# Performance work log

Hardware: AMD Instinct MI355X
Metric: run time of the kernel (lower is better)

The kernel has to match this reference:

```python
import jax, jax.numpy as jnp
import numpy as np

# Config (matches AttentionConfig)
B, T, D = 2, 2048, 2048
H, KV, HD = 32, 8, 64          # n_heads, n_kv_heads, head_dim = d_model // n_heads
GROUPS = H // KV               # 4 query heads share each KV head
THETA = 10000.0
SCALE = 1.0 / np.sqrt(HD)
EPS = 1e-6


def setup_inputs() -> dict:
    key = jax.random.key(0)
    ks = jax.random.split(key, 6)
    def xavier(k, fan_in, fan_out):
        limit = np.sqrt(6.0 / (fan_in + fan_out))
        return jax.random.uniform(k, (fan_in, fan_out), jnp.float32, -limit, limit)
    return {
        "x": jax.random.normal(ks[0], (B, T, D), jnp.float32),
        "Wq": xavier(ks[1], D, H * HD),
        "Wk": xavier(ks[2], D, KV * HD),
        "Wv": xavier(ks[3], D, KV * HD),
        "Wo": xavier(ks[4], H * HD, D),
        "q_scale": jnp.ones((HD,), jnp.float32),
        "k_scale": jnp.ones((HD,), jnp.float32),
    }


def _rmsnorm(x, scale):
    # per-head RMSNorm over last dim (head_dim)
    rms = jnp.sqrt(jnp.mean(jnp.square(x), axis=-1, keepdims=True) + EPS)
    return (x / rms) * scale


def _rope(x):
    # x: (B, T, h, HD); rotate-half RoPE, offset=0
    pos = jnp.arange(x.shape[1], dtype=jnp.float32)
    inv_freq = 1.0 / (THETA ** (jnp.arange(0, HD, 2, dtype=jnp.float32) / HD))
    ang = pos[:, None] * inv_freq[None, :]          # (T, HD/2)
    cos = jnp.cos(ang)[None, :, None, :]
    sin = jnp.sin(ang)[None, :, None, :]
    x1, x2 = x[..., : HD // 2], x[..., HD // 2 :]
    return jnp.concatenate([x1 * cos - x2 * sin, x2 * cos + x1 * sin], axis=-1)


def reference(x, Wq, Wk, Wv, Wo, q_scale, k_scale):
    # projections -> (B, T, heads, HD)
    q = (x @ Wq).reshape(B, T, H, HD)
    k = (x @ Wk).reshape(B, T, KV, HD)
    v = (x @ Wv).reshape(B, T, KV, HD)
    # per-head QK RMSNorm (applied before RoPE, as in the module)
    q = _rmsnorm(q, q_scale)
    k = _rmsnorm(k, k_scale)
    # RoPE on q and k
    q = _rope(q)
    k = _rope(k)
    # repeat KV heads: head index = kv_head * GROUPS + g (matches _repeat_kv)
    k = jnp.repeat(k, GROUPS, axis=2)   # (B, T, H, HD)
    v = jnp.repeat(v, GROUPS, axis=2)
    # attention scores (B, H, T, T)
    logits = jnp.einsum("bqhd,bkhd->bhqk", q, k) * SCALE
    causal = jnp.triu(jnp.ones((T, T), bool), k=1)  # True = masked
    logits = jnp.where(causal[None, None], -jnp.inf, logits)
    w = jax.nn.softmax(logits, axis=-1)
    w = jnp.nan_to_num(w)
    out = jnp.einsum("bhqk,bkhd->bqhd", w, v).reshape(B, T, H * HD)
    return out @ Wo
```

## Files before the change

kernel.cpp:

```cpp
#include <hip/hip_runtime.h>
#include <hip/hip_bf16.h>

typedef __attribute__((ext_vector_type(4))) float f32x4;
typedef __attribute__((ext_vector_type(8))) short bf16x8;
typedef __attribute__((ext_vector_type(4))) short short4v;

#define DEVI __device__ __forceinline__

constexpr int Bc = 2, Tc = 2048, Dc = 2048, Hc = 32, KVc = 8, HDc = 64;
constexpr int GRP = Hc / KVc;
constexpr float EPSc = 1e-6f;
constexpr float QMULT = 0.125f * 1.4426950408889634f;
constexpr float INV2PI = 0.15915494309189535f;
constexpr float ROPE_C = 0.41524101186092029f;

DEVI short f2b(float f) {
    __hip_bfloat16 h = __float2bfloat16(f);
    short s;
    __builtin_memcpy(&s, &h, sizeof(short));
    return s;
}
DEVI float b2f(short s) {
    unsigned int u = ((unsigned int)(unsigned short)s) << 16;
    float f;
    __builtin_memcpy(&f, &u, sizeof(float));
    return f;
}

#define GLOAD16(g, l)                                                        \
    __builtin_amdgcn_global_load_lds(                                        \
        (const __attribute__((address_space(1))) void*)(g),                  \
        (__attribute__((address_space(3))) void*)(l), 16, 0, 0)

__global__ __launch_bounds__(256) void prep_all(const float* __restrict__ x,
                                                const float* __restrict__ Wq,
                                                const float* __restrict__ Wk,
                                                const float* __restrict__ Wv,
                                                const float* __restrict__ Wo,
                                                short* __restrict__ xb,
                                                short* __restrict__ WqkvT,
                                                short* __restrict__ WoT) {
    const int z = blockIdx.z;
    if (z == 4) {
        size_t base = ((size_t)(blockIdx.y * 32 + blockIdx.x) * 256 + threadIdx.x) * 8;
#pragma unroll
        for (int p = 0; p < 4; ++p) {
            size_t i = base + (size_t)p * 2097152;
            float4 a = *reinterpret_cast<const float4*>(x + i);
            float4 b = *reinterpret_cast<const float4*>(x + i + 4);
            bf16x8 o = {f2b(a.x), f2b(a.y), f2b(a.z), f2b(a.w),
                        f2b(b.x), f2b(b.y), f2b(b.z), f2b(b.w)};
            *reinterpret_cast<bf16x8*>(xb + i) = o;
        }
        return;
    }
    const float* src;
    short* dst;
    int C;
    if (z == 0)      { src = Wq; dst = WqkvT;                          C = 2048; }
    else if (z == 1) { src = Wk; dst = WqkvT + (size_t)2048 * 2048;    C = 512; }
    else if (z == 2) { src = Wv; dst = WqkvT + (size_t)2560 * 2048;    C = 512; }
    else             { src = Wo; dst = WoT;                            C = 2048; }
    const int n0 = blockIdx.x * 64, k0 = blockIdx.y * 64;
    if (n0 >= C) return;

    __shared__ __align__(16) short t[64][72];
    const int rl = threadIdx.x >> 2, q = threadIdx.x & 3;
#pragma unroll
    for (int jj = 0; jj < 4; ++jj) {
        float4 v = *reinterpret_cast<const float4*>(src + (size_t)(k0 + rl) * C + n0 + q * 16 + jj * 4);
        short4v s = {f2b(v.x), f2b(v.y), f2b(v.z), f2b(v.w)};
        *reinterpret_cast<short4v*>(&t[rl][q * 16 + jj * 4]) = s;
    }
    __syncthreads();
    alignas(16) short buf[16];
#pragma unroll
    for (int e = 0; e < 16; ++e) buf[e] = t[q * 16 + e][rl];
    short* d = dst + (size_t)(n0 + rl) * 2048 + k0 + q * 16;
    *reinterpret_cast<int4*>(d) = reinterpret_cast<int4*>(buf)[0];
    *reinterpret_cast<int4*>(d + 8) = reinterpret_cast<int4*>(buf)[1];
}

DEVI void xcd_swizzle(int nx, int& bx, int& by) {
    int nwg = nx * gridDim.y;
    int fb = by * nx + bx;
    int cpx = nwg >> 3;
    int swz = (fb & 7) * cpx + (fb >> 3);
    by = swz / nx;
    bx = swz - by * nx;
}

__global__ __launch_bounds__(256) void gemm_proj(const short* __restrict__ A,
                                                 const short* __restrict__ Bt,
                                                 const float* __restrict__ qs,
                                                 const float* __restrict__ ks,
                                                 short* __restrict__ qb,
                                                 short* __restrict__ kb,
                                                 short* __restrict__ vslab) {
    constexpr int K = 2048;
    __shared__ __align__(16) short sA[2][128 * 64];
    __shared__ __align__(16) short sB[2][128 * 64];

    const int tid = threadIdx.x;
    const int wave = tid >> 6, lane = tid & 63;
    const int lhi = lane >> 4, llo = lane & 15;
    int bx = blockIdx.x, by = blockIdx.y;
    xcd_swizzle(24, bx, by);
    const int bm = by * 128, bn = bx * 128;
    const int wm = (wave >> 1) * 64, wn = (wave & 1) * 64;

    const short* apt[4];
    const short* bpt[4];
#pragma unroll
    for (int l = 0; l < 4; ++l) {
        int c = l * 256 + tid;
        int r = c >> 3, ck = (c & 7) ^ (r & 7);
        apt[l] = A + (size_t)(bm + r) * K + ck * 8;
        bpt[l] = Bt + (size_t)(bn + r) * K + ck * 8;
    }

    f32x4 acc[4][4] = {};

#pragma unroll
    for (int l = 0; l < 4; ++l) {
        GLOAD16(apt[l], &sA[0][(l * 256 + tid) * 8]);
        GLOAD16(bpt[l], &sB[0][(l * 256 + tid) * 8]);
    }
    int c = 0;
    const int co0 = ((lhi ^ (llo & 7)) << 3);
    const int co1 = (((4 + lhi) ^ (llo & 7)) << 3);

#pragma unroll 1
    for (int k0 = 0; k0 < K; k0 += 64) {
        if (k0 + 64 < K) {
            const int kn = k0 + 64;
#pragma unroll
            for (int l = 0; l < 4; ++l) {
                GLOAD16(apt[l] + kn, &sA[c ^ 1][(l * 256 + tid) * 8]);
                GLOAD16(bpt[l] + kn, &sB[c ^ 1][(l * 256 + tid) * 8]);
            }
            asm volatile("s_waitcnt vmcnt(8)" ::: "memory");
        } else {
            asm volatile("s_waitcnt vmcnt(0)" ::: "memory");
        }
        __builtin_amdgcn_s_barrier();
        asm volatile("" ::: "memory");

#pragma unroll
        for (int kk = 0; kk < 2; ++kk) {
            const int co = kk ? co1 : co0;
            bf16x8 af[4], bf[4];
#pragma unroll
            for (int i = 0; i < 4; ++i)
                af[i] = *reinterpret_cast<const bf16x8*>(&sA[c][(wm + i * 16 + llo) * 64 + co]);
#pragma unroll
            for (int j = 0; j < 4; ++j)
                bf[j] = *reinterpret_cast<const bf16x8*>(&sB[c][(wn + j * 16 + llo) * 64 + co]);
#pragma unroll
            for (int i = 0; i < 4; ++i)
#pragma unroll
                for (int j = 0; j < 4; ++j)
                    acc[i][j] = __builtin_amdgcn_mfma_f32_16x16x32_bf16(af[i], bf[j], acc[i][j], 0, 0, 0);
        }

        asm volatile("" ::: "memory");
        __builtin_amdgcn_s_barrier();
        c ^= 1;
    }

    const int rm = bm + wm;
    const int b = rm >> 11;
    const int tb = rm & 2047;
    const int col0 = bn + wn;

    if (col0 < 2560) {
        const bool isq = col0 < 2048;
        const float* scale = isq ? qs : ks;
        const float mult = isq ? QMULT : 1.0f;
        float scl[4];
#pragma unroll
        for (int j = 0; j < 4; ++j) scl[j] = scale[j * 16 + llo];
        short* outp;
        if (isq)
            outp = qb + (size_t)(b * Hc + (col0 >> 6)) * 2048 * 64;
        else
            outp = kb + (size_t)(b * KVc + ((col0 - 2048) >> 6)) * 2048 * 64;
        const float ir0 = INV2PI * exp2f(-ROPE_C * (float)llo);
        const float ir1 = INV2PI * exp2f(-ROPE_C * (float)(16 + llo));
#pragma unroll
        for (int i = 0; i < 4; ++i)
#pragma unroll
            for (int r = 0; r < 4; ++r) {
                float ss = 0.f;
#pragma unroll
                for (int j = 0; j < 4; ++j) ss += acc[i][j][r] * acc[i][j][r];
                ss += __shfl_xor(ss, 1);
                ss += __shfl_xor(ss, 2);
                ss += __shfl_xor(ss, 4);
                ss += __shfl_xor(ss, 8);
                float rinv = 1.0f / sqrtf(ss * (1.0f / 64.0f) + EPSc);
                float vn[4];
#pragma unroll
                for (int j = 0; j < 4; ++j) vn[j] = acc[i][j][r] * rinv * scl[j];
                const int t = tb + i * 16 + lhi * 4 + r;
                float f0 = (float)t * ir0;
                f0 -= floorf(f0);
                float f1 = (float)t * ir1;
                f1 -= floorf(f1);
                float sn0 = __builtin_amdgcn_sinf(f0), cs0 = __builtin_amdgcn_cosf(f0);
                float sn1 = __builtin_amdgcn_sinf(f1), cs1 = __builtin_amdgcn_cosf(f1);
                size_t base = (size_t)t * 64 + llo;
                outp[base]      = f2b((vn[0] * cs0 - vn[2] * sn0) * mult);
                outp[base + 16] = f2b((vn[1] * cs1 - vn[3] * sn1) * mult);
                outp[base + 32] = f2b((vn[2] * cs0 + vn[0] * sn0) * mult);
                outp[base + 48] = f2b((vn[3] * cs1 + vn[1] * sn1) * mult);
            }
    } else {
        const int cb = col0 - 2560;
#pragma unroll
        for (int i = 0; i < 4; ++i)
#pragma unroll
            for (int j = 0; j < 4; ++j)
#pragma unroll
                for (int r = 0; r < 4; ++r)
                    vslab[(size_t)(rm + i * 16 + lhi * 4 + r) * 512 + cb + j * 16 + llo] =
                        f2b(acc[i][j][r]);
    }
}

template <typename CT>
__global__ __launch_bounds__(256) void gemm_bt(const short* __restrict__ A,
                                               const short* __restrict__ Bt,
                                               CT* __restrict__ C, int M, int N, int K) {
    __shared__ __align__(16) short sA[2][128 * 64];
    __shared__ __align__(16) short sB[2][128 * 64];

    const int tid = threadIdx.x;
    const int wave = tid >> 6, lane = tid & 63;
    const int lhi = lane >> 4, llo = lane & 15;
    int bx = blockIdx.x, by = blockIdx.y;
    xcd_swizzle(gridDim.x, bx, by);
    const int bm = by * 128, bn = bx * 128;
    const int wm = (wave >> 1) * 64, wn = (wave & 1) * 64;

    const short* apt[4];
    const short* bpt[4];
#pragma unroll
    for (int l = 0; l < 4; ++l) {
        int c = l * 256 + tid;
        int r = c >> 3, ck = (c & 7) ^ (r & 7);
        apt[l] = A + (size_t)(bm + r) * K + ck * 8;
        bpt[l] = Bt + (size_t)(bn + r) * K + ck * 8;
    }

    f32x4 acc[4][4] = {};

#pragma unroll
    for (int l = 0; l < 4; ++l) {
        GLOAD16(apt[l], &sA[0][(l * 256 + tid) * 8]);
        GLOAD16(bpt[l], &sB[0][(l * 256 + tid) * 8]);
    }
    int c = 0;
    const int co0 = ((lhi ^ (llo & 7)) << 3);
    const int co1 = (((4 + lhi) ^ (llo & 7)) << 3);

#pragma unroll 1
    for (int k0 = 0; k0 < K; k0 += 64) {
        if (k0 + 64 < K) {
            const int kn = k0 + 64;
#pragma unroll
            for (int l = 0; l < 4; ++l) {
                GLOAD16(apt[l] + kn, &sA[c ^ 1][(l * 256 + tid) * 8]);
                GLOAD16(bpt[l] + kn, &sB[c ^ 1][(l * 256 + tid) * 8]);
            }
            asm volatile("s_waitcnt vmcnt(8)" ::: "memory");
        } else {
            asm volatile("s_waitcnt vmcnt(0)" ::: "memory");
        }
        __builtin_amdgcn_s_barrier();
        asm volatile("" ::: "memory");

#pragma unroll
        for (int kk = 0; kk < 2; ++kk) {
            const int co = kk ? co1 : co0;
            bf16x8 af[4], bf[4];
#pragma unroll
            for (int i = 0; i < 4; ++i)
                af[i] = *reinterpret_cast<const bf16x8*>(&sA[c][(wm + i * 16 + llo) * 64 + co]);
#pragma unroll
            for (int j = 0; j < 4; ++j)
                bf[j] = *reinterpret_cast<const bf16x8*>(&sB[c][(wn + j * 16 + llo) * 64 + co]);
#pragma unroll
            for (int i = 0; i < 4; ++i)
#pragma unroll
                for (int j = 0; j < 4; ++j)
                    acc[i][j] = __builtin_amdgcn_mfma_f32_16x16x32_bf16(af[i], bf[j], acc[i][j], 0, 0, 0);
        }

        asm volatile("" ::: "memory");
        __builtin_amdgcn_s_barrier();
        c ^= 1;
    }

#pragma unroll
    for (int i = 0; i < 4; ++i)
#pragma unroll
        for (int j = 0; j < 4; ++j)
#pragma unroll
            for (int r = 0; r < 4; ++r) {
                size_t idx = (size_t)(bm + wm + i * 16 + lhi * 4 + r) * N + bn + wn + j * 16 + llo;
                if constexpr (sizeof(CT) == 2)
                    C[idx] = f2b(acc[i][j][r]);
                else
                    C[idx] = acc[i][j][r];
            }
}

__global__ __launch_bounds__(256) void fuse_vt(const short* __restrict__ vsrc,
                                               short* __restrict__ vt, int ldin) {
    __shared__ __align__(16) short t[64][72];
    const int tile = blockIdx.x, kv = blockIdx.y, b = blockIdx.z;
    const int tl = threadIdx.x >> 2, q = threadIdx.x & 3;
    const short* src = vsrc + (size_t)(b * 2048 + tile * 64 + tl) * ldin + kv * 64 + q * 16;
    *reinterpret_cast<bf16x8*>(&t[tl][q * 16]) = *reinterpret_cast<const bf16x8*>(src);
    *reinterpret_cast<bf16x8*>(&t[tl][q * 16 + 8]) = *reinterpret_cast<const bf16x8*>(src + 8);
    __syncthreads();
    alignas(16) short buf[16];
#pragma unroll
    for (int e = 0; e < 16; ++e) buf[e] = t[q * 16 + e][tl];
    short* dst = vt + ((size_t)(b * 8 + kv) * 32 + tile) * 4096 + tl * 64 + q * 16;
    *reinterpret_cast<int4*>(dst) = reinterpret_cast<int4*>(buf)[0];
    *reinterpret_cast<int4*>(dst + 8) = reinterpret_cast<int4*>(buf)[1];
}

__global__ __launch_bounds__(256) void attn_fwd(const short* __restrict__ Qb,
                                                const short* __restrict__ Kb,
                                                const short* __restrict__ Vt,
                                                short* __restrict__ Ob) {
    __shared__ __align__(16) short sK[2][64 * 64];
    __shared__ __align__(16) short sV[2][64 * 64];
    __shared__ __align__(16) short sP[4][32 * 72];

    const int pair = blockIdx.x;
    const int h = blockIdx.y, b = blockIdx.z;
    const int kvh = h >> 2;
    const int tid = threadIdx.x, wave = tid >> 6, lane = tid & 63;
    const int lhi = lane >> 4, llo = lane & 15;

    const short* Qp = Qb + (size_t)(b * Hc + h) * Tc * 64;
    const short* Kp = Kb + (size_t)(b * KVc + kvh) * Tc * 64;
    const short* Vp = Vt + (size_t)(b * KVc + kvh) * 32 * 4096;

    const int srow0 = tid >> 3, sslot0 = tid & 7;
    const int srow1 = (256 + tid) >> 3, sslot1 = tid & 7;
    const int soff0 = (sslot0 ^ (srow0 & 7)) * 8;
    const int soff1 = (sslot1 ^ (srow1 & 7)) * 8;

#pragma unroll 1
    for (int sub = 0; sub < 2; ++sub) {
        const int qt = sub ? pair : 15 - pair;
        const int Q0 = qt * 128 + wave * 32;
        const int ktmax_w = (Q0 + 31) >> 6;
        const int nkt = 2 * qt + 2;

        bf16x8 qf[2][2];
#pragma unroll
        for (int q16 = 0; q16 < 2; ++q16)
#pragma unroll
            for (int kk = 0; kk < 2; ++kk)
                qf[q16][kk] = *reinterpret_cast<const bf16x8*>(
                    Qp + (size_t)(Q0 + q16 * 16 + llo) * 64 + kk * 32 + lhi * 8);

        f32x4 o[2][4] = {};
        float mreg[2] = {-1e30f, -1e30f};
        float lreg[2] = {0.f, 0.f};

        {
            GLOAD16(Kp + (size_t)srow0 * 64 + soff0, &sK[0][tid * 8]);
            GLOAD16(Vp + (size_t)srow0 * 64 + soff0, &sV[0][tid * 8]);
            GLOAD16(Kp + (size_t)srow1 * 64 + soff1, &sK[0][(256 + tid) * 8]);
            GLOAD16(Vp + (size_t)srow1 * 64 + soff1, &sV[0][(256 + tid) * 8]);
        }
        int c = 0;

#pragma unroll 1
        for (int kt = 0; kt < nkt; ++kt) {
            const bool has_next = (kt + 1) < nkt;
            if (has_next) {
                const size_t kbase = (size_t)(kt + 1) * 4096;
                GLOAD16(Kp + kbase + srow0 * 64 + soff0, &sK[c ^ 1][tid * 8]);
                GLOAD16(Vp + kbase + srow0 * 64 + soff0, &sV[c ^ 1][tid * 8]);
                GLOAD16(Kp + kbase + srow1 * 64 + soff1, &sK[c ^ 1][(256 + tid) * 8]);
                GLOAD16(Vp + kbase + srow1 * 64 + soff1, &sV[c ^ 1][(256 + tid) * 8]);
                asm volatile("s_waitcnt vmcnt(4)" ::: "memory");
            } else {
                asm volatile("s_waitcnt vmcnt(0)" ::: "memory");
            }
            __builtin_amdgcn_s_barrier();
            asm volatile("" ::: "memory");

            if (kt <= ktmax_w) {
                const short* sKc = sK[c];
                const short* sVc = sV[c];
                f32x4 st[2][4];
#pragma unroll
                for (int n = 0; n < 4; ++n) {
                    int krow = n * 16 + llo;
                    bf16x8 ka0 = *reinterpret_cast<const bf16x8*>(
                        &sKc[krow * 64 + ((lhi ^ (krow & 7)) << 3)]);
                    bf16x8 ka1 = *reinterpret_cast<const bf16x8*>(
                        &sKc[krow * 64 + (((4 + lhi) ^ (krow & 7)) << 3)]);
                    f32x4 z = {0.f, 0.f, 0.f, 0.f};
                    st[0][n] = __builtin_amdgcn_mfma_f32_16x16x32_bf16(ka0, qf[0][0], z, 0, 0, 0);
                    st[0][n] = __builtin_amdgcn_mfma_f32_16x16x32_bf16(ka1, qf[0][1], st[0][n], 0, 0, 0);
                    st[1][n] = __builtin_amdgcn_mfma_f32_16x16x32_bf16(ka0, qf[1][0], z, 0, 0, 0);
                    st[1][n] = __builtin_amdgcn_mfma_f32_16x16x32_bf16(ka1, qf[1][1], st[1][n], 0, 0, 0);
                }
                if (kt == ktmax_w) {
#pragma unroll
                    for (int q16 = 0; q16 < 2; ++q16) {
                        int qg = Q0 + q16 * 16 + llo;
#pragma unroll
                        for (int n = 0; n < 4; ++n)
#pragma unroll
                            for (int r = 0; r < 4; ++r) {
                                int kvg = kt * 64 + n * 16 + lhi * 4 + r;
                                if (kvg > qg) st[q16][n][r] = -1e30f;
                            }
                    }
                }
                float pm[2];
#pragma unroll
                for (int q16 = 0; q16 < 2; ++q16) {
                    float p = st[q16][0][0];
#pragma unroll
                    for (int n = 0; n < 4; ++n)
#pragma unroll
                        for (int r = 0; r < 4; ++r) p = fmaxf(p, st[q16][n][r]);
                    p = fmaxf(p, __shfl_xor(p, 16));
                    p = fmaxf(p, __shfl_xor(p, 32));
                    pm[q16] = p;
                }
                bool defer = __all((pm[0] - mreg[0] <= 8.f) && (pm[1] - mreg[1] <= 8.f));
                if (!defer) {
                    float alpha[2];
#pragma unroll
                    for (int q16 = 0; q16 < 2; ++q16) {
                        float mn = fmaxf(mreg[q16], pm[q16]);
                        alpha[q16] = __builtin_amdgcn_exp2f(mreg[q16] - mn);
                        mreg[q16] = mn;
                        lreg[q16] *= alpha[q16];
                    }
#pragma unroll
                    for (int q16 = 0; q16 < 2; ++q16)
#pragma unroll
                        for (int r = 0; r < 4; ++r) {
                            float ar = __shfl(alpha[q16], lhi * 4 + r);
#pragma unroll
                            for (int j = 0; j < 4; ++j) o[q16][j][r] *= ar;
                        }
                }
#pragma unroll
                for (int q16 = 0; q16 < 2; ++q16) {
                    float ps = 0.f;
#pragma unroll
                    for (int n = 0; n < 4; ++n)
#pragma unroll
                        for (int r = 0; r < 4; ++r) {
                            float p = __builtin_amdgcn_exp2f(st[q16][n][r] - mreg[q16]);
                            st[q16][n][r] = p;
                            ps += p;
                        }
                    ps += __shfl_xor(ps, 16);
                    ps += __shfl_xor(ps, 32);
                    lreg[q16] += ps;
                }
#pragma unroll
                for (int q16 = 0; q16 < 2; ++q16)
#pragma unroll
                    for (int n = 0; n < 4; ++n) {
                        short4v p4 = {f2b(st[q16][n][0]), f2b(st[q16][n][1]),
                                      f2b(st[q16][n][2]), f2b(st[q16][n][3])};
                        *reinterpret_cast<short4v*>(
                            &sP[wave][(q16 * 16 + llo) * 72 + n * 16 + lhi * 4]) = p4;
                    }
#pragma unroll
                for (int kk = 0; kk < 2; ++kk) {
                    bf16x8 pa0 = *reinterpret_cast<const bf16x8*>(
                        &sP[wave][(0 * 16 + llo) * 72 + kk * 32 + lhi * 8]);
                    bf16x8 pa1 = *reinterpret_cast<const bf16x8*>(
                        &sP[wave][(1 * 16 + llo) * 72 + kk * 32 + lhi * 8]);
#pragma unroll
                    for (int j = 0; j < 4; ++j) {
                        int vrow = j * 16 + llo;
                        bf16x8 vf = *reinterpret_cast<const bf16x8*>(
                            &sVc[vrow * 64 + ((((kk * 4) + lhi) ^ (vrow & 7)) << 3)]);
                        o[0][j] = __builtin_amdgcn_mfma_f32_16x16x32_bf16(pa0, vf, o[0][j], 0, 0, 0);
                        o[1][j] = __builtin_amdgcn_mfma_f32_16x16x32_bf16(pa1, vf, o[1][j], 0, 0, 0);
                    }
                }
            }
            asm volatile("" ::: "memory");
            __builtin_amdgcn_s_barrier();
            c ^= 1;
        }

#pragma unroll
        for (int q16 = 0; q16 < 2; ++q16) {
            float inv = 1.0f / lreg[q16];
#pragma unroll
            for (int r = 0; r < 4; ++r) {
                float ivr = __shfl(inv, lhi * 4 + r);
                int qrow = Q0 + q16 * 16 + lhi * 4 + r;
#pragma unroll
                for (int j = 0; j < 4; ++j)
                    Ob[((size_t)(b * Tc + qrow)) * 2048 + h * 64 + j * 16 + llo] =
                        f2b(o[q16][j][r] * ivr);
            }
        }
    }
}

extern "C" void kernel_launch(void* const* d_in, const int* in_sizes, int n_in,
                              void* d_out, int out_size, void* d_ws, size_t ws_size,
                              hipStream_t stream) {
    const float* x  = (const float*)d_in[0];
    const float* Wq = (const float*)d_in[1];
    const float* Wk = (const float*)d_in[2];
    const float* Wv = (const float*)d_in[3];
    const float* Wo = (const float*)d_in[4];
    const float* qs = (const float*)d_in[5];
    const float* ks = (const float*)d_in[6];
    float* out = (float*)d_out;

    char* w = (char*)d_ws;
    short* xb    = (short*)(w);
    short* WqkvT = (short*)(w + 16777216);
    short* WoT   = (short*)(w + 29360128);
    short* vslab = (short*)(w + 37748736);
    short* qb    = (short*)(w + 62914560);
    short* kb    = (short*)(w + 79691776);
    short* vt    = WqkvT;
    short* ob    = xb;

    dim3 blk(256);
    prep_all<<<dim3(32, 32, 5), blk, 0, stream>>>(x, Wq, Wk, Wv, Wo, xb, WqkvT, WoT);
    gemm_proj<<<dim3(24, 32), blk, 0, stream>>>(xb, WqkvT, qs, ks, qb, kb, vslab);
    fuse_vt<<<dim3(32, 8, 2), blk, 0, stream>>>(vslab, vt, 512);
    attn_fwd<<<dim3(8, 32, 2), blk, 0, stream>>>(qb, kb, vt, ob);
    gemm_bt<float><<<dim3(16, 32), blk, 0, stream>>>(ob, WoT, out, 4096, 2048, 2048);
}
```

Baseline: 222.8 us.

## Fuse V transpose into projection epilogue, add MFMA priority, tree max reduction

The projection GEMM epilogue now writes V directly in the transposed per-tile layout that attention consumes, so the separate fuse_vt kernel launch and its extra global round trip are removed. The attention kernel raises wave priority around its MFMA blocks with s_setprio, and the row max is computed as a balanced tree instead of a serial chain. The epilogue writes become short4 scattered stores with a stride of 64 elements, which may coalesce poorly.

```diff
diff --git a/kernel.cpp b/kernel.cpp
--- a/kernel.cpp
+++ b/kernel.cpp
@@ -96,7 +96,7 @@
                                                  const float* __restrict__ ks,
                                                  short* __restrict__ qb,
                                                  short* __restrict__ kb,
-                                                 short* __restrict__ vslab) {
+                                                 short* __restrict__ vt) {
     constexpr int K = 2048;
     __shared__ __align__(16) short sA[2][128 * 64];
     __shared__ __align__(16) short sB[2][128 * 64];
@@ -216,15 +216,18 @@
                 outp[base + 48] = f2b((vn[3] * cs1 + vn[1] * sn1) * mult);
             }
     } else {
-        const int cb = col0 - 2560;
+        const int kv = (col0 - 2560) >> 6;
+        const int tile = tb >> 6;
+        short* dst = vt + ((size_t)(b * 8 + kv) * 32 + tile) * 4096;
 #pragma unroll
         for (int i = 0; i < 4; ++i)
 #pragma unroll
-            for (int j = 0; j < 4; ++j)
-#pragma unroll
-                for (int r = 0; r < 4; ++r)
-                    vslab[(size_t)(rm + i * 16 + lhi * 4 + r) * 512 + cb + j * 16 + llo] =
-                        f2b(acc[i][j][r]);
+            for (int j = 0; j < 4; ++j) {
+                short4v p4 = {f2b(acc[i][j][0]), f2b(acc[i][j][1]),
+                              f2b(acc[i][j][2]), f2b(acc[i][j][3])};
+                *reinterpret_cast<short4v*>(
+                    &dst[(j * 16 + llo) * 64 + i * 16 + lhi * 4]) = p4;
+            }
     }
 }
 
@@ -314,23 +317,6 @@
                 else
                     C[idx] = acc[i][j][r];
             }
-}
-
-__global__ __launch_bounds__(256) void fuse_vt(const short* __restrict__ vsrc,
-                                               short* __restrict__ vt, int ldin) {
-    __shared__ __align__(16) short t[64][72];
-    const int tile = blockIdx.x, kv = blockIdx.y, b = blockIdx.z;
-    const int tl = threadIdx.x >> 2, q = threadIdx.x & 3;
-    const short* src = vsrc + (size_t)(b * 2048 + tile * 64 + tl) * ldin + kv * 64 + q * 16;
-    *reinterpret_cast<bf16x8*>(&t[tl][q * 16]) = *reinterpret_cast<const bf16x8*>(src);
-    *reinterpret_cast<bf16x8*>(&t[tl][q * 16 + 8]) = *reinterpret_cast<const bf16x8*>(src + 8);
-    __syncthreads();
-    alignas(16) short buf[16];
-#pragma unroll
-    for (int e = 0; e < 16; ++e) buf[e] = t[q * 16 + e][tl];
-    short* dst = vt + ((size_t)(b * 8 + kv) * 32 + tile) * 4096 + tl * 64 + q * 16;
-    *reinterpret_cast<int4*>(dst) = reinterpret_cast<int4*>(buf)[0];
-    *reinterpret_cast<int4*>(dst + 8) = reinterpret_cast<int4*>(buf)[1];
 }
 
 __global__ __launch_bounds__(256) void attn_fwd(const short* __restrict__ Qb,
@@ -403,6 +389,7 @@
                 const short* sKc = sK[c];
                 const short* sVc = sV[c];
                 f32x4 st[2][4];
+                __builtin_amdgcn_s_setprio(1);
 #pragma unroll
                 for (int n = 0; n < 4; ++n) {
                     int krow = n * 16 + llo;
@@ -416,6 +403,7 @@
                     st[1][n] = __builtin_amdgcn_mfma_f32_16x16x32_bf16(ka0, qf[1][0], z, 0, 0, 0);
                     st[1][n] = __builtin_amdgcn_mfma_f32_16x16x32_bf16(ka1, qf[1][1], st[1][n], 0, 0, 0);
                 }
+                __builtin_amdgcn_s_setprio(0);
                 if (kt == ktmax_w) {
 #pragma unroll
                     for (int q16 = 0; q16 < 2; ++q16) {
@@ -432,11 +420,15 @@
                 float pm[2];
 #pragma unroll
                 for (int q16 = 0; q16 < 2; ++q16) {
-                    float p = st[q16][0][0];
-#pragma unroll
-                    for (int n = 0; n < 4; ++n)
-#pragma unroll
-                        for (int r = 0; r < 4; ++r) p = fmaxf(p, st[q16][n][r]);
+                    float r0 = fmaxf(fmaxf(st[q16][0][0], st[q16][0][1]),
+                                     fmaxf(st[q16][0][2], st[q16][0][3]));
+                    float r1 = fmaxf(fmaxf(st[q16][1][0], st[q16][1][1]),
+                                     fmaxf(st[q16][1][2], st[q16][1][3]));
+                    float r2 = fmaxf(fmaxf(st[q16][2][0], st[q16][2][1]),
+                                     fmaxf(st[q16][2][2], st[q16][2][3]));
+                    float r3 = fmaxf(fmaxf(st[q16][3][0], st[q16][3][1]),
+                                     fmaxf(st[q16][3][2], st[q16][3][3]));
+                    float p = fmaxf(fmaxf(r0, r1), fmaxf(r2, r3));
                     p = fmaxf(p, __shfl_xor(p, 16));
                     p = fmaxf(p, __shfl_xor(p, 32));
                     pm[q16] = p;
@@ -484,6 +476,7 @@
                         *reinterpret_cast<short4v*>(
                             &sP[wave][(q16 * 16 + llo) * 72 + n * 16 + lhi * 4]) = p4;
                     }
+                __builtin_amdgcn_s_setprio(1);
 #pragma unroll
                 for (int kk = 0; kk < 2; ++kk) {
                     bf16x8 pa0 = *reinterpret_cast<const bf16x8*>(
@@ -499,6 +492,7 @@
                         o[1][j] = __builtin_amdgcn_mfma_f32_16x16x32_bf16(pa1, vf, o[1][j], 0, 0, 0);
                     }
                 }
+                __builtin_amdgcn_s_setprio(0);
             }
             asm volatile("" ::: "memory");
             __builtin_amdgcn_s_barrier();
@@ -537,16 +531,14 @@
     short* xb    = (short*)(w);
     short* WqkvT = (short*)(w + 16777216);
     short* WoT   = (short*)(w + 29360128);
-    short* vslab = (short*)(w + 37748736);
+    short* vt    = (short*)(w + 37748736);
     short* qb    = (short*)(w + 62914560);
     short* kb    = (short*)(w + 79691776);
-    short* vt    = WqkvT;
     short* ob    = xb;
 
     dim3 blk(256);
     prep_all<<<dim3(32, 32, 5), blk, 0, stream>>>(x, Wq, Wk, Wv, Wo, xb, WqkvT, WoT);
-    gemm_proj<<<dim3(24, 32), blk, 0, stream>>>(xb, WqkvT, qs, ks, qb, kb, vslab);
-    fuse_vt<<<dim3(32, 8, 2), blk, 0, stream>>>(vslab, vt, 512);
+    gemm_proj<<<dim3(24, 32), blk, 0, stream>>>(xb, WqkvT, qs, ks, qb, kb, vt);
     attn_fwd<<<dim3(8, 32, 2), blk, 0, stream>>>(qb, kb, vt, ob);
     gemm_bt<float><<<dim3(16, 32), blk, 0, stream>>>(ob, WoT, out, 4096, 2048, 2048);
 }
```

Result: no change. 220.0 us (-1.2%).
